# Kernel tuning notes

Hardware: AMD Instinct MI355X
Metric: run time of the kernel (lower is better)

Reference implementation:

```python
import jax, jax.numpy as jnp
import numpy as np

B, S, E, H, D = 2, 2048, 1024, 16, 64  # batch, seq(=max_seq_len), embed_dim, heads, atten_dim


def setup_inputs() -> dict:
    key = jax.random.key(0)
    ks = jax.random.split(key, 9)
    s = 0.02
    return {
        "x": jax.random.normal(ks[0], (B, S, E), jnp.float32),
        "Wq": jax.random.normal(ks[1], (H, E, D), jnp.float32) * s,
        "Wk": jax.random.normal(ks[2], (H, E, D), jnp.float32) * s,
        "Wv": jax.random.normal(ks[3], (H, E, D), jnp.float32) * s,
        "bq": jax.random.normal(ks[4], (H, D), jnp.float32) * s,
        "bk": jax.random.normal(ks[5], (H, D), jnp.float32) * s,
        "bv": jax.random.normal(ks[6], (H, D), jnp.float32) * s,
        "Wp": jax.random.normal(ks[7], (H * D, E), jnp.float32) * s,
        "bp": jax.random.normal(ks[8], (E,), jnp.float32) * s,
    }


def reference(x, Wq, Wk, Wv, bq, bk, bv, Wp, bp):
    scale = jnp.sqrt(jnp.float32(D))
    # per-head projections, all heads at once: [B,H,S,D]
    q = jnp.einsum("bse,hed->bhsd", x, Wq) + bq[:, None, :]
    k = jnp.einsum("bse,hed->bhsd", x, Wk) + bk[:, None, :]
    v = jnp.einsum("bse,hed->bhsd", x, Wv) + bv[:, None, :]
    # causal scores [B,H,S,S], additive -inf mask above diagonal (as in the buffer)
    score = jnp.einsum("bhsd,bhtd->bhst", q, k) / scale
    mask = jnp.triu(jnp.full((S, S), -jnp.inf, jnp.float32), k=1)
    score = score + mask
    probs = jax.nn.softmax(score, axis=-1)
    attn = jnp.einsum("bhst,bhtd->bhsd", probs, v)
    # concat heads -> [B,S,H*D], then projection + ReLU
    concat = attn.transpose(0, 2, 1, 3).reshape(B, S, H * D)
    out = jax.nn.relu(concat @ Wp + bp)
    return out
```

## Files before the change

kernel.cpp:

```cpp
#include <hip/hip_runtime.h>

#define S_LEN 2048
#define E_DIM 1024
#define H_NUM 16
#define D_DIM 64

typedef unsigned short u16;
using bf16x8 = __attribute__((ext_vector_type(8))) short;
using f32x4  = __attribute__((ext_vector_type(4))) float;

#define MFMA16(A, B, C) __builtin_amdgcn_mfma_f32_16x16x32_bf16(A, B, C, 0, 0, 0)

__device__ __forceinline__ u16 f2bf(float f) {
    unsigned u = __float_as_uint(f);
    u += 0x7fffu + ((u >> 16) & 1u);
    return (u16)(u >> 16);
}
__device__ __forceinline__ f32x4 fzero4() { f32x4 z; z[0]=0.f; z[1]=0.f; z[2]=0.f; z[3]=0.f; return z; }

__device__ __forceinline__ void gll16(const u16* g, u16* l) {
    __builtin_amdgcn_global_load_lds(
        (const __attribute__((address_space(1))) void*)g,
        (__attribute__((address_space(3))) void*)l, 16, 0, 0);
}

__global__ __launch_bounds__(256) void cvt_bf16(const float* __restrict__ in, u16* __restrict__ outp, int n) {
    int i4 = (blockIdx.x * 256 + threadIdx.x) * 4;
    if (i4 < n) {
        float4 f = *(const float4*)(in + i4);
        unsigned lo = (unsigned)f2bf(f.x) | ((unsigned)f2bf(f.y) << 16);
        unsigned hi = (unsigned)f2bf(f.z) | ((unsigned)f2bf(f.w) << 16);
        uint2 p; p.x = lo; p.y = hi;
        *(uint2*)(outp + i4) = p;
    }
}

__device__ __forceinline__ void cvt_t_tile(const float* __restrict__ bin, u16* __restrict__ bout,
                                           int R, int C, int r0, int c0) {
    __shared__ float t[64][65];
    const int tid = threadIdx.x;
    const int lr = tid >> 2, lc = (tid & 3) * 16;

    const float* src = bin + (size_t)(r0 + lr) * C + c0 + lc;
    #pragma unroll
    for (int j = 0; j < 4; j++) {
        float4 f = *(const float4*)(src + j * 4);
        t[lr][lc + j * 4 + 0] = f.x; t[lr][lc + j * 4 + 1] = f.y;
        t[lr][lc + j * 4 + 2] = f.z; t[lr][lc + j * 4 + 3] = f.w;
    }
    __syncthreads();

    u16* dst = bout + (size_t)(c0 + lr) * R + r0 + lc;
    u16 vals[16];
    #pragma unroll
    for (int i = 0; i < 16; i++) vals[i] = f2bf(t[lc + i][lr]);
    uint4 pa, pb;
    pa.x = vals[0] | (vals[1] << 16);  pa.y = vals[2] | (vals[3] << 16);
    pa.z = vals[4] | (vals[5] << 16);  pa.w = vals[6] | (vals[7] << 16);
    pb.x = vals[8] | (vals[9] << 16);  pb.y = vals[10] | (vals[11] << 16);
    pb.z = vals[12] | (vals[13] << 16); pb.w = vals[14] | (vals[15] << 16);
    *(uint4*)dst = pa;
    *(uint4*)(dst + 8) = pb;
}

__global__ __launch_bounds__(256) void cvt_bf16_t(const float* __restrict__ in, u16* __restrict__ outp,
                                                  int R, int C) {
    const float* bin = in + (size_t)blockIdx.z * R * C;
    u16* bout = outp + (size_t)blockIdx.z * R * C;
    cvt_t_tile(bin, bout, R, C, blockIdx.y * 64, blockIdx.x * 64);
}

__global__ __launch_bounds__(256) void cvt_w3_t(
    const float* __restrict__ Wq, const float* __restrict__ Wk, const float* __restrict__ Wv,
    u16* __restrict__ wqt, u16* __restrict__ wkt, u16* __restrict__ wvt) {
    const int which = blockIdx.z >> 4, bh = blockIdx.z & 15;
    const float* in = (which == 0) ? Wq : (which == 1) ? Wk : Wv;
    u16* outp = (which == 0) ? wqt : (which == 1) ? wkt : wvt;
    const float* bin = in + (size_t)bh * E_DIM * D_DIM;
    u16* bout = outp + (size_t)bh * E_DIM * D_DIM;
    cvt_t_tile(bin, bout, E_DIM, D_DIM, blockIdx.y * 64, 0);
}

__global__ __launch_bounds__(256) void vt_prep(const u16* __restrict__ v, u16* __restrict__ vt) {
    const int st = blockIdx.x;
    const int bhi = blockIdx.y;
    __shared__ u16 t[64 * 72];
    const int tid = threadIdx.x;
    const int wave = tid >> 6, lane = tid & 63;

    const u16* src = v + (size_t)bhi * S_LEN * D_DIM + (size_t)(st * 64 + lane) * D_DIM + wave * 16;
    uint4 a = *(const uint4*)(src);
    uint4 b = *(const uint4*)(src + 8);
    unsigned w[8] = { a.x, a.y, a.z, a.w, b.x, b.y, b.z, b.w };
    #pragma unroll
    for (int j = 0; j < 8; j++) {
        t[(wave * 16 + 2 * j    ) * 72 + lane] = (u16)(w[j] & 0xffffu);
        t[(wave * 16 + 2 * j + 1) * 72 + lane] = (u16)(w[j] >> 16);
    }
    __syncthreads();

    const int dr = tid >> 2, sc = (tid & 3) * 16;
    u16* dst = vt + (size_t)bhi * D_DIM * S_LEN + (size_t)dr * S_LEN + st * 64 + sc;
    *(uint4*)(dst    ) = *(const uint4*)(&t[dr * 72 + sc    ]);
    *(uint4*)(dst + 8) = *(const uint4*)(&t[dr * 72 + sc + 8]);
}

__global__ __launch_bounds__(256) void qkv_gemm(
    const u16* __restrict__ xb, const u16* __restrict__ wcat,
    const float* __restrict__ bq, const float* __restrict__ bk, const float* __restrict__ bv,
    u16* __restrict__ oq, u16* __restrict__ okk, u16* __restrict__ ov)
{
    const int m0 = blockIdx.x * 128;
    const int n0 = blockIdx.y * 128;

    __shared__ u16 As[128 * 32];
    __shared__ u16 Bs[128 * 32];

    const int tid  = threadIdx.x;
    const int wave = tid >> 6, lane = tid & 63, quad = lane >> 4, l16 = lane & 15;
    const int mh = wave >> 1, nh = wave & 1;

    const int lrow = lane >> 2, lcol = (lane & 3) * 8;
    const u16* aBase = xb   + (size_t)(m0 + wave * 32 + lrow) * E_DIM + lcol;
    const u16* bBase = wcat + (size_t)(n0 + wave * 32 + lrow) * E_DIM + lcol;
    u16* aLds0 = &As[(wave * 32     ) * 32];
    u16* aLds1 = &As[(wave * 32 + 16) * 32];
    u16* bLds0 = &Bs[(wave * 32     ) * 32];
    u16* bLds1 = &Bs[(wave * 32 + 16) * 32];

    f32x4 acc[4][4];
    #pragma unroll
    for (int j = 0; j < 4; j++)
        #pragma unroll
        for (int mi = 0; mi < 4; mi++) acc[j][mi] = fzero4();

    for (int k0 = 0; k0 < E_DIM; k0 += 32) {
        __syncthreads();
        gll16(aBase + k0,                 aLds0);
        gll16(aBase + k0 + 16 * E_DIM,    aLds1);
        gll16(bBase + k0,                 bLds0);
        gll16(bBase + k0 + 16 * E_DIM,    bLds1);
        __syncthreads();

        bf16x8 af[4];
        #pragma unroll
        for (int mi = 0; mi < 4; mi++)
            af[mi] = *(const bf16x8*)(&As[(mh * 64 + mi * 16 + l16) * 32 + quad * 8]);
        #pragma unroll
        for (int j = 0; j < 4; j++) {
            bf16x8 bfv = *(const bf16x8*)(&Bs[(nh * 64 + j * 16 + l16) * 32 + quad * 8]);
            #pragma unroll
            for (int mi = 0; mi < 4; mi++)
                acc[j][mi] = MFMA16(af[mi], bfv, acc[j][mi]);
        }
    }

    u16* outp[3] = { oq, okk, ov };
    const float* biasp[3] = { bq, bk, bv };
    #pragma unroll
    for (int j = 0; j < 4; j++) {
        const int n = n0 + nh * 64 + j * 16 + l16;
        const int t = n >> 10, h = (n >> 6) & 15, d = n & 63;
        float bia = biasp[t][h * D_DIM + d];
        const float scl = (t == 0) ? 0.125f : 1.0f;
        u16* dst = outp[t];
        #pragma unroll
        for (int mi = 0; mi < 4; mi++) {
            #pragma unroll
            for (int r = 0; r < 4; r++) {
                int m = m0 + mh * 64 + mi * 16 + quad * 4 + r;
                int b = m >> 11, s = m & 2047;
                dst[((size_t)(b * H_NUM + h) * S_LEN + s) * D_DIM + d] =
                    f2bf((acc[j][mi][r] + bia) * scl);
            }
        }
    }
}

__global__ __launch_bounds__(256) void attn_fwd(
    const u16* __restrict__ q, const u16* __restrict__ k, const u16* __restrict__ vt,
    u16* __restrict__ concat)
{
    const int p  = blockIdx.x;
    const int qa = p, qb = 31 - p;
    const int h  = blockIdx.y;
    const int bb = blockIdx.z;

    const size_t headoff = (size_t)(bb * H_NUM + h) * S_LEN * D_DIM;
    const u16* qh  = q  + headoff;
    const u16* kh  = k  + headoff;
    const u16* vth = vt + headoff;

    __shared__ u16 Qa[64 * 72];
    __shared__ u16 Qb[64 * 72];
    __shared__ u16 Ks[64 * 72];
    __shared__ u16 Vts[64 * 72];
    __shared__ u16 Ps[4][16 * 72];

    const int tid  = threadIdx.x;
    const int wave = tid >> 6, lane = tid & 63, quad = lane >> 4, l16 = lane & 15;

    const int srow = tid >> 2, scg = tid & 3;

    {
        const u16* qsa = qh + (size_t)(qa * 64 + srow) * D_DIM + scg * 16;
        const u16* qsb = qh + (size_t)(qb * 64 + srow) * D_DIM + scg * 16;
        *(uint4*)(&Qa[srow * 72 + scg * 16    ]) = *(const uint4*)(qsa);
        *(uint4*)(&Qa[srow * 72 + scg * 16 + 8]) = *(const uint4*)(qsa + 8);
        *(uint4*)(&Qb[srow * 72 + scg * 16    ]) = *(const uint4*)(qsb);
        *(uint4*)(&Qb[srow * 72 + scg * 16 + 8]) = *(const uint4*)(qsb + 8);
    }
    __syncthreads();

    bf16x8 bqa0 = *(const bf16x8*)(&Qa[(wave * 16 + l16) * 72 + quad * 8]);
    bf16x8 bqa1 = *(const bf16x8*)(&Qa[(wave * 16 + l16) * 72 + 32 + quad * 8]);
    bf16x8 bqb0 = *(const bf16x8*)(&Qb[(wave * 16 + l16) * 72 + quad * 8]);
    bf16x8 bqb1 = *(const bf16x8*)(&Qb[(wave * 16 + l16) * 72 + 32 + quad * 8]);

    f32x4 oa[4], ob[4];
    #pragma unroll
    for (int nt = 0; nt < 4; nt++) { oa[nt] = fzero4(); ob[nt] = fzero4(); }
    float la = 0.f, lb = 0.f;

    uint4 kA, kB, vA, vB;
    {
        const u16* ksrc = kh + (size_t)srow * D_DIM + scg * 16;
        kA = *(const uint4*)(ksrc); kB = *(const uint4*)(ksrc + 8);
        const u16* vsrc = vth + (size_t)srow * S_LEN + scg * 16;
        vA = *(const uint4*)(vsrc); vB = *(const uint4*)(vsrc + 8);
    }

    const int qga = qa * 64 + wave * 16 + l16;
    const int qgb = qb * 64 + wave * 16 + l16;

    for (int kt = 0; kt <= qb; kt++) {
        __syncthreads();
        *(uint4*)(&Ks[srow * 72 + scg * 16    ]) = kA;
        *(uint4*)(&Ks[srow * 72 + scg * 16 + 8]) = kB;
        *(uint4*)(&Vts[srow * 72 + scg * 16    ]) = vA;
        *(uint4*)(&Vts[srow * 72 + scg * 16 + 8]) = vB;
        __syncthreads();

        if (kt < qb) {
            const u16* ksrc = kh + (size_t)((kt + 1) * 64 + srow) * D_DIM + scg * 16;
            kA = *(const uint4*)(ksrc); kB = *(const uint4*)(ksrc + 8);
            const u16* vsrc = vth + (size_t)srow * S_LEN + (kt + 1) * 64 + scg * 16;
            vA = *(const uint4*)(vsrc); vB = *(const uint4*)(vsrc + 8);
        }

        const bool both = (kt <= qa);

        f32x4 stb[4], sta[4];
        #pragma unroll
        for (int nt = 0; nt < 4; nt++) {
            bf16x8 ak0 = *(const bf16x8*)(&Ks[(nt * 16 + l16) * 72 + quad * 8]);
            bf16x8 ak1 = *(const bf16x8*)(&Ks[(nt * 16 + l16) * 72 + 32 + quad * 8]);
            stb[nt] = fzero4();
            stb[nt] = MFMA16(ak0, bqb0, stb[nt]);
            stb[nt] = MFMA16(ak1, bqb1, stb[nt]);
            if (both) {
                sta[nt] = fzero4();
                sta[nt] = MFMA16(ak0, bqa0, sta[nt]);
                sta[nt] = MFMA16(ak1, bqa1, sta[nt]);
            }
        }

        {
            u16* pw = &Ps[wave][0];
            #pragma unroll
            for (int nt = 0; nt < 4; nt++) {
                float pe[4];
                if (kt == qb) {
                    #pragma unroll
                    for (int r = 0; r < 4; r++) {
                        int kkg = kt * 64 + nt * 16 + quad * 4 + r;
                        pe[r] = (kkg > qgb) ? 0.f : __expf(stb[nt][r]);
                    }
                } else {
                    #pragma unroll
                    for (int r = 0; r < 4; r++) pe[r] = __expf(stb[nt][r]);
                }
                lb += pe[0] + pe[1] + pe[2] + pe[3];
                uint2 pk;
                pk.x = (unsigned)f2bf(pe[0]) | ((unsigned)f2bf(pe[1]) << 16);
                pk.y = (unsigned)f2bf(pe[2]) | ((unsigned)f2bf(pe[3]) << 16);
                *(uint2*)(&pw[l16 * 72 + nt * 16 + quad * 4]) = pk;
            }
            bf16x8 ap0 = *(const bf16x8*)(&Ps[wave][l16 * 72 + quad * 8]);
            bf16x8 ap1 = *(const bf16x8*)(&Ps[wave][l16 * 72 + 32 + quad * 8]);
            #pragma unroll
            for (int nt = 0; nt < 4; nt++) {
                bf16x8 bv0 = *(const bf16x8*)(&Vts[(nt * 16 + l16) * 72 + quad * 8]);
                bf16x8 bv1 = *(const bf16x8*)(&Vts[(nt * 16 + l16) * 72 + 32 + quad * 8]);
                ob[nt] = MFMA16(ap0, bv0, ob[nt]);
                ob[nt] = MFMA16(ap1, bv1, ob[nt]);
            }
        }

        if (both) {
            u16* pw = &Ps[wave][0];
            #pragma unroll
            for (int nt = 0; nt < 4; nt++) {
                float pe[4];
                if (kt == qa) {
                    #pragma unroll
                    for (int r = 0; r < 4; r++) {
                        int kkg = kt * 64 + nt * 16 + quad * 4 + r;
                        pe[r] = (kkg > qga) ? 0.f : __expf(sta[nt][r]);
                    }
                } else {
                    #pragma unroll
                    for (int r = 0; r < 4; r++) pe[r] = __expf(sta[nt][r]);
                }
                la += pe[0] + pe[1] + pe[2] + pe[3];
                uint2 pk;
                pk.x = (unsigned)f2bf(pe[0]) | ((unsigned)f2bf(pe[1]) << 16);
                pk.y = (unsigned)f2bf(pe[2]) | ((unsigned)f2bf(pe[3]) << 16);
                *(uint2*)(&pw[l16 * 72 + nt * 16 + quad * 4]) = pk;
            }
            bf16x8 ap0 = *(const bf16x8*)(&Ps[wave][l16 * 72 + quad * 8]);
            bf16x8 ap1 = *(const bf16x8*)(&Ps[wave][l16 * 72 + 32 + quad * 8]);
            #pragma unroll
            for (int nt = 0; nt < 4; nt++) {
                bf16x8 bv0 = *(const bf16x8*)(&Vts[(nt * 16 + l16) * 72 + quad * 8]);
                bf16x8 bv1 = *(const bf16x8*)(&Vts[(nt * 16 + l16) * 72 + 32 + quad * 8]);
                oa[nt] = MFMA16(ap0, bv0, oa[nt]);
                oa[nt] = MFMA16(ap1, bv1, oa[nt]);
            }
        }
    }

    lb += __shfl_xor(lb, 16); lb += __shfl_xor(lb, 32);
    la += __shfl_xor(la, 16); la += __shfl_xor(la, 32);

    #pragma unroll
    for (int r = 0; r < 4; r++) {
        const int srcl = quad * 4 + r;
        float lbr = __shfl(lb, srcl);
        float lar = __shfl(la, srcl);
        int sqa = qa * 64 + wave * 16 + quad * 4 + r;
        int sqb = qb * 64 + wave * 16 + quad * 4 + r;
        #pragma unroll
        for (int nt = 0; nt < 4; nt++) {
            concat[((size_t)(bb * S_LEN + sqa)) * E_DIM + h * D_DIM + nt * 16 + l16] =
                f2bf(oa[nt][r] / lar);
            concat[((size_t)(bb * S_LEN + sqb)) * E_DIM + h * D_DIM + nt * 16 + l16] =
                f2bf(ob[nt][r] / lbr);
        }
    }
}

__global__ __launch_bounds__(256) void out_proj(
    const u16* __restrict__ concat, const u16* __restrict__ wpt,
    const float* __restrict__ bp, float* __restrict__ out)
{
    const int m0 = blockIdx.x * 128;
    const int n0 = blockIdx.y * 128;

    __shared__ u16 As[128 * 40];
    __shared__ u16 Bs[128 * 40];

    const int tid  = threadIdx.x;
    const int wave = tid >> 6, lane = tid & 63, quad = lane >> 4, l16 = lane & 15;
    const int mh = wave >> 1, nh = wave & 1;

    const int arow = tid >> 1, acol = (tid & 1) * 16;

    const u16* aptr = concat + (size_t)(m0 + arow) * E_DIM + acol;
    const u16* bptr = wpt + (size_t)(n0 + arow) * E_DIM + acol;

    f32x4 acc[4][4];
    #pragma unroll
    for (int j = 0; j < 4; j++)
        #pragma unroll
        for (int mi = 0; mi < 4; mi++) acc[j][mi] = fzero4();

    uint4 pA0, pA1, pB0, pB1;
    pA0 = *(const uint4*)(aptr);     pA1 = *(const uint4*)(aptr + 8);
    pB0 = *(const uint4*)(bptr);     pB1 = *(const uint4*)(bptr + 8);

    for (int k0 = 0; k0 < E_DIM; k0 += 32) {
        __syncthreads();
        *(uint4*)(&As[arow * 40 + acol    ]) = pA0;
        *(uint4*)(&As[arow * 40 + acol + 8]) = pA1;
        *(uint4*)(&Bs[arow * 40 + acol    ]) = pB0;
        *(uint4*)(&Bs[arow * 40 + acol + 8]) = pB1;
        __syncthreads();

        if (k0 + 32 < E_DIM) {
            pA0 = *(const uint4*)(aptr + k0 + 32);  pA1 = *(const uint4*)(aptr + k0 + 40);
            pB0 = *(const uint4*)(bptr + k0 + 32);  pB1 = *(const uint4*)(bptr + k0 + 40);
        }

        bf16x8 af[4];
        #pragma unroll
        for (int mi = 0; mi < 4; mi++)
            af[mi] = *(const bf16x8*)(&As[(mh * 64 + mi * 16 + l16) * 40 + quad * 8]);
        #pragma unroll
        for (int j = 0; j < 4; j++) {
            bf16x8 bfv = *(const bf16x8*)(&Bs[(nh * 64 + j * 16 + l16) * 40 + quad * 8]);
            #pragma unroll
            for (int mi = 0; mi < 4; mi++)
                acc[j][mi] = MFMA16(af[mi], bfv, acc[j][mi]);
        }
    }

    #pragma unroll
    for (int j = 0; j < 4; j++) {
        int n = n0 + nh * 64 + j * 16 + l16;
        float bia = bp[n];
        #pragma unroll
        for (int mi = 0; mi < 4; mi++) {
            #pragma unroll
            for (int r = 0; r < 4; r++) {
                int m = m0 + mh * 64 + mi * 16 + quad * 4 + r;
                out[(size_t)m * E_DIM + n] = fmaxf(acc[j][mi][r] + bia, 0.f);
            }
        }
    }
}

extern "C" void kernel_launch(void* const* d_in, const int* in_sizes, int n_in,
                              void* d_out, int out_size, void* d_ws, size_t ws_size,
                              hipStream_t stream)
{
    (void)in_sizes; (void)n_in; (void)out_size; (void)ws_size;
    const float* x  = (const float*)d_in[0];
    const float* Wq = (const float*)d_in[1];
    const float* Wk = (const float*)d_in[2];
    const float* Wv = (const float*)d_in[3];
    const float* bq = (const float*)d_in[4];
    const float* bk = (const float*)d_in[5];
    const float* bv = (const float*)d_in[6];
    const float* Wp = (const float*)d_in[7];
    const float* bp = (const float*)d_in[8];
    float* out = (float*)d_out;

    const size_t QKV_ELEMS = (size_t)2 * H_NUM * S_LEN * D_DIM;
    const size_t W_ELEMS   = (size_t)H_NUM * E_DIM * D_DIM;

    u16* q   = (u16*)d_ws;
    u16* k   = q   + QKV_ELEMS;
    u16* v   = k   + QKV_ELEMS;
    u16* cc  = v   + QKV_ELEMS;
    u16* xb  = cc  + QKV_ELEMS;
    u16* wqt = xb  + QKV_ELEMS;
    u16* wkt = wqt + W_ELEMS;
    u16* wvt = wkt + W_ELEMS;
    u16* wpt = wvt + W_ELEMS;
    u16* vtr = xb;

    cvt_bf16<<<dim3(4096), 256, 0, stream>>>(x, xb, (int)QKV_ELEMS);
    cvt_w3_t<<<dim3(1, 16, 48), 256, 0, stream>>>(Wq, Wk, Wv, wqt, wkt, wvt);
    cvt_bf16_t<<<dim3(16, 16, 1), 256, 0, stream>>>(Wp, wpt, H_NUM * D_DIM, E_DIM);

    qkv_gemm<<<dim3(32, 24), 256, 0, stream>>>(xb, wqt, bq, bk, bv, q, k, v);
    vt_prep<<<dim3(32, 32), 256, 0, stream>>>(v, vtr);
    attn_fwd<<<dim3(16, 16, 2), 256, 0, stream>>>(q, k, vtr, cc);
    out_proj<<<dim3(32, 8), 256, 0, stream>>>(cc, wpt, bp, out);
}
```

Before: 200.4 us.

## Split attention KV range across two blocks and merge partials in out_proj

Attention now splits each query tile's causal KV range into two halves processed by separate blocks (split-K). This doubles the grid and launch_bounds requests 4 blocks per SM for higher occupancy. Unnormalised bf16 partial outputs and row sums go to workspace, and out_proj merges and normalises them while loading its A operand. The kernel also uses exp2 with log2e folded into the Q scale, a truncating bf16 pack for P, XOR-swizzled LDS, and double-buffered async global->LDS loads for K/V. The cost is extra workspace traffic for the partials, added merge arithmetic in out_proj, and some rounding of partial results to bf16.

```diff
diff --git a/kernel.cpp b/kernel.cpp
--- a/kernel.cpp
+++ b/kernel.cpp
@@ -16,6 +16,10 @@
     u += 0x7fffu + ((u >> 16) & 1u);
     return (u16)(u >> 16);
 }
+__device__ __forceinline__ unsigned pack_bf16_tr(float lo, float hi) {
+    return (__float_as_uint(lo) >> 16) | (__float_as_uint(hi) & 0xffff0000u);
+}
+__device__ __forceinline__ float bfu(unsigned u) { return __uint_as_float(u << 16); }
 __device__ __forceinline__ f32x4 fzero4() { f32x4 z; z[0]=0.f; z[1]=0.f; z[2]=0.f; z[3]=0.f; return z; }
 
 __device__ __forceinline__ void gll16(const u16* g, u16* l) {
@@ -155,6 +159,7 @@
         }
     }
 
+    const float QSCL = 0.125f * 1.44269504089f;
     u16* outp[3] = { oq, okk, ov };
     const float* biasp[3] = { bq, bk, bv };
     #pragma unroll
@@ -162,7 +167,7 @@
         const int n = n0 + nh * 64 + j * 16 + l16;
         const int t = n >> 10, h = (n >> 6) & 15, d = n & 63;
         float bia = biasp[t][h * D_DIM + d];
-        const float scl = (t == 0) ? 0.125f : 1.0f;
+        const float scl = (t == 0) ? QSCL : 1.0f;
         u16* dst = outp[t];
         #pragma unroll
         for (int mi = 0; mi < 4; mi++) {
@@ -177,12 +182,13 @@
     }
 }
 
-__global__ __launch_bounds__(256) void attn_fwd(
+__global__ __launch_bounds__(256, 4) void attn_split(
     const u16* __restrict__ q, const u16* __restrict__ k, const u16* __restrict__ vt,
-    u16* __restrict__ concat)
+    u16* __restrict__ op0, u16* __restrict__ op1,
+    float* __restrict__ ls0, float* __restrict__ ls1)
 {
-    const int p  = blockIdx.x;
-    const int qa = p, qb = 31 - p;
+    const int x = blockIdx.x;
+    const int p = x & 15, half = x >> 4;
     const int h  = blockIdx.y;
     const int bb = blockIdx.z;
 
@@ -191,168 +197,140 @@
     const u16* kh  = k  + headoff;
     const u16* vth = vt + headoff;
 
-    __shared__ u16 Qa[64 * 72];
-    __shared__ u16 Qb[64 * 72];
-    __shared__ u16 Ks[64 * 72];
-    __shared__ u16 Vts[64 * 72];
-    __shared__ u16 Ps[4][16 * 72];
+    u16*   opart = half ? op1 : op0;
+    float* lsum  = half ? ls1 : ls0;
+
+    __shared__ u16 Ks[2][64 * 64];
+    __shared__ u16 Vts[2][64 * 64];
+    __shared__ u16 QP[64 * 64];
 
     const int tid  = threadIdx.x;
     const int wave = tid >> 6, lane = tid & 63, quad = lane >> 4, l16 = lane & 15;
-
     const int srow = tid >> 2, scg = tid & 3;
 
-    {
-        const u16* qsa = qh + (size_t)(qa * 64 + srow) * D_DIM + scg * 16;
-        const u16* qsb = qh + (size_t)(qb * 64 + srow) * D_DIM + scg * 16;
-        *(uint4*)(&Qa[srow * 72 + scg * 16    ]) = *(const uint4*)(qsa);
-        *(uint4*)(&Qa[srow * 72 + scg * 16 + 8]) = *(const uint4*)(qsa + 8);
-        *(uint4*)(&Qb[srow * 72 + scg * 16    ]) = *(const uint4*)(qsb);
-        *(uint4*)(&Qb[srow * 72 + scg * 16 + 8]) = *(const uint4*)(qsb + 8);
-    }
-    __syncthreads();
-
-    bf16x8 bqa0 = *(const bf16x8*)(&Qa[(wave * 16 + l16) * 72 + quad * 8]);
-    bf16x8 bqa1 = *(const bf16x8*)(&Qa[(wave * 16 + l16) * 72 + 32 + quad * 8]);
-    bf16x8 bqb0 = *(const bf16x8*)(&Qb[(wave * 16 + l16) * 72 + quad * 8]);
-    bf16x8 bqb1 = *(const bf16x8*)(&Qb[(wave * 16 + l16) * 72 + 32 + quad * 8]);
-
-    f32x4 oa[4], ob[4];
-    #pragma unroll
-    for (int nt = 0; nt < 4; nt++) { oa[nt] = fzero4(); ob[nt] = fzero4(); }
-    float la = 0.f, lb = 0.f;
-
-    uint4 kA, kB, vA, vB;
-    {
-        const u16* ksrc = kh + (size_t)srow * D_DIM + scg * 16;
-        kA = *(const uint4*)(ksrc); kB = *(const uint4*)(ksrc + 8);
-        const u16* vsrc = vth + (size_t)srow * S_LEN + scg * 16;
-        vA = *(const uint4*)(vsrc); vB = *(const uint4*)(vsrc + 8);
-    }
-
-    const int qga = qa * 64 + wave * 16 + l16;
-    const int qgb = qb * 64 + wave * 16 + l16;
-
-    for (int kt = 0; kt <= qb; kt++) {
+    const int gr = wave * 8 + (lane >> 3);
+    const int gc = lane & 7;
+    const int cl = gc ^ (gr & 7);
+    const u16* kbase = kh  + (size_t)gr * D_DIM + cl * 8;
+    const u16* vbase = vth + (size_t)gr * S_LEN + cl * 8;
+    u16* kl0[2] = { &Ks[0][wave * 512], &Ks[1][wave * 512] };
+    u16* kl1[2] = { &Ks[0][2048 + wave * 512], &Ks[1][2048 + wave * 512] };
+    u16* vl0[2] = { &Vts[0][wave * 512], &Vts[1][wave * 512] };
+    u16* vl1[2] = { &Vts[0][2048 + wave * 512], &Vts[1][2048 + wave * 512] };
+
+    const int sx_lo = ((quad    ) ^ (l16 & 7)) * 8;
+    const int sx_hi = ((quad + 4) ^ (l16 & 7)) * 8;
+    int psw[4];
+    #pragma unroll
+    for (int nt = 0; nt < 4; nt++)
+        psw[nt] = wave * 1024 + l16 * 64 + (((nt * 2 + (quad >> 1)) ^ (l16 & 7)) * 8) + (quad & 1) * 4;
+
+    const int qw = wave * 16 + l16;
+
+    #pragma unroll 1
+    for (int seg = 0; seg < 2; seg++) {
+        const int qt = seg ? (31 - p) : p;
+        const int n  = qt + 1;
+        const int r0 = half ? ((n + 1) >> 1) : 0;
+        const int r1 = half ? n : ((n + 1) >> 1);
+        const int nIt = r1 - r0;
+
         __syncthreads();
-        *(uint4*)(&Ks[srow * 72 + scg * 16    ]) = kA;
-        *(uint4*)(&Ks[srow * 72 + scg * 16 + 8]) = kB;
-        *(uint4*)(&Vts[srow * 72 + scg * 16    ]) = vA;
-        *(uint4*)(&Vts[srow * 72 + scg * 16 + 8]) = vB;
-        __syncthreads();
-
-        if (kt < qb) {
-            const u16* ksrc = kh + (size_t)((kt + 1) * 64 + srow) * D_DIM + scg * 16;
-            kA = *(const uint4*)(ksrc); kB = *(const uint4*)(ksrc + 8);
-            const u16* vsrc = vth + (size_t)srow * S_LEN + (kt + 1) * 64 + scg * 16;
-            vA = *(const uint4*)(vsrc); vB = *(const uint4*)(vsrc + 8);
-        }
-
-        const bool both = (kt <= qa);
-
-        f32x4 stb[4], sta[4];
-        #pragma unroll
-        for (int nt = 0; nt < 4; nt++) {
-            bf16x8 ak0 = *(const bf16x8*)(&Ks[(nt * 16 + l16) * 72 + quad * 8]);
-            bf16x8 ak1 = *(const bf16x8*)(&Ks[(nt * 16 + l16) * 72 + 32 + quad * 8]);
-            stb[nt] = fzero4();
-            stb[nt] = MFMA16(ak0, bqb0, stb[nt]);
-            stb[nt] = MFMA16(ak1, bqb1, stb[nt]);
-            if (both) {
-                sta[nt] = fzero4();
-                sta[nt] = MFMA16(ak0, bqa0, sta[nt]);
-                sta[nt] = MFMA16(ak1, bqa1, sta[nt]);
-            }
+        if (nIt > 0) {
+            gll16(kbase + (size_t)r0 * 4096,                       kl0[0]);
+            gll16(kbase + (size_t)r0 * 4096 + 2048,                kl1[0]);
+            gll16(vbase + (size_t)r0 * 64,                         vl0[0]);
+            gll16(vbase + (size_t)r0 * 64 + (size_t)32 * S_LEN,    vl1[0]);
         }
 
         {
-            u16* pw = &Ps[wave][0];
+            const u16* qs = qh + (size_t)(qt * 64 + srow) * D_DIM + scg * 16;
+            *(uint4*)(&QP[srow * 64 + (((scg * 2    ) ^ (srow & 7)) * 8)]) = *(const uint4*)(qs);
+            *(uint4*)(&QP[srow * 64 + (((scg * 2 + 1) ^ (srow & 7)) * 8)]) = *(const uint4*)(qs + 8);
+        }
+        bf16x8 bq0 = *(const bf16x8*)(&QP[(wave * 16 + l16) * 64 + sx_lo]);
+        bf16x8 bq1 = *(const bf16x8*)(&QP[(wave * 16 + l16) * 64 + sx_hi]);
+
+        f32x4 o[4];
+        #pragma unroll
+        for (int nt = 0; nt < 4; nt++) o[nt] = fzero4();
+        float lsv = 0.f;
+
+        const int qg = qt * 64 + qw;
+
+        for (int i = 0; i < nIt; i++) {
+            const int kt = r0 + i;
+            const u16* ksb = &Ks[i & 1][0];
+            const u16* vsb = &Vts[i & 1][0];
+            __syncthreads();
+
+            if (i + 1 < nIt) {
+                const int nb = (i + 1) & 1;
+                gll16(kbase + (size_t)(kt + 1) * 4096,                    kl0[nb]);
+                gll16(kbase + (size_t)(kt + 1) * 4096 + 2048,             kl1[nb]);
+                gll16(vbase + (size_t)(kt + 1) * 64,                      vl0[nb]);
+                gll16(vbase + (size_t)(kt + 1) * 64 + (size_t)32 * S_LEN, vl1[nb]);
+            }
+
+            f32x4 st[4];
+            #pragma unroll
+            for (int nt = 0; nt < 4; nt++) {
+                bf16x8 ak0 = *(const bf16x8*)(&ksb[(nt * 16 + l16) * 64 + sx_lo]);
+                bf16x8 ak1 = *(const bf16x8*)(&ksb[(nt * 16 + l16) * 64 + sx_hi]);
+                st[nt] = fzero4();
+                st[nt] = MFMA16(ak0, bq0, st[nt]);
+                st[nt] = MFMA16(ak1, bq1, st[nt]);
+            }
+
             #pragma unroll
             for (int nt = 0; nt < 4; nt++) {
                 float pe[4];
-                if (kt == qb) {
+                if (kt == qt) {
                     #pragma unroll
                     for (int r = 0; r < 4; r++) {
                         int kkg = kt * 64 + nt * 16 + quad * 4 + r;
-                        pe[r] = (kkg > qgb) ? 0.f : __expf(stb[nt][r]);
+                        pe[r] = (kkg > qg) ? 0.f : exp2f(st[nt][r]);
                     }
                 } else {
                     #pragma unroll
-                    for (int r = 0; r < 4; r++) pe[r] = __expf(stb[nt][r]);
+                    for (int r = 0; r < 4; r++) pe[r] = exp2f(st[nt][r]);
                 }
-                lb += pe[0] + pe[1] + pe[2] + pe[3];
+                lsv += pe[0] + pe[1] + pe[2] + pe[3];
                 uint2 pk;
-                pk.x = (unsigned)f2bf(pe[0]) | ((unsigned)f2bf(pe[1]) << 16);
-                pk.y = (unsigned)f2bf(pe[2]) | ((unsigned)f2bf(pe[3]) << 16);
-                *(uint2*)(&pw[l16 * 72 + nt * 16 + quad * 4]) = pk;
-            }
-            bf16x8 ap0 = *(const bf16x8*)(&Ps[wave][l16 * 72 + quad * 8]);
-            bf16x8 ap1 = *(const bf16x8*)(&Ps[wave][l16 * 72 + 32 + quad * 8]);
+                pk.x = pack_bf16_tr(pe[0], pe[1]);
+                pk.y = pack_bf16_tr(pe[2], pe[3]);
+                *(uint2*)(&QP[psw[nt]]) = pk;
+            }
+
+            bf16x8 ap0 = *(const bf16x8*)(&QP[wave * 1024 + l16 * 64 + sx_lo]);
+            bf16x8 ap1 = *(const bf16x8*)(&QP[wave * 1024 + l16 * 64 + sx_hi]);
             #pragma unroll
             for (int nt = 0; nt < 4; nt++) {
-                bf16x8 bv0 = *(const bf16x8*)(&Vts[(nt * 16 + l16) * 72 + quad * 8]);
-                bf16x8 bv1 = *(const bf16x8*)(&Vts[(nt * 16 + l16) * 72 + 32 + quad * 8]);
-                ob[nt] = MFMA16(ap0, bv0, ob[nt]);
-                ob[nt] = MFMA16(ap1, bv1, ob[nt]);
-            }
-        }
-
-        if (both) {
-            u16* pw = &Ps[wave][0];
-            #pragma unroll
-            for (int nt = 0; nt < 4; nt++) {
-                float pe[4];
-                if (kt == qa) {
-                    #pragma unroll
-                    for (int r = 0; r < 4; r++) {
-                        int kkg = kt * 64 + nt * 16 + quad * 4 + r;
-                        pe[r] = (kkg > qga) ? 0.f : __expf(sta[nt][r]);
-                    }
-                } else {
-                    #pragma unroll
-                    for (int r = 0; r < 4; r++) pe[r] = __expf(sta[nt][r]);
-                }
-                la += pe[0] + pe[1] + pe[2] + pe[3];
-                uint2 pk;
-                pk.x = (unsigned)f2bf(pe[0]) | ((unsigned)f2bf(pe[1]) << 16);
-                pk.y = (unsigned)f2bf(pe[2]) | ((unsigned)f2bf(pe[3]) << 16);
-                *(uint2*)(&pw[l16 * 72 + nt * 16 + quad * 4]) = pk;
-            }
-            bf16x8 ap0 = *(const bf16x8*)(&Ps[wave][l16 * 72 + quad * 8]);
-            bf16x8 ap1 = *(const bf16x8*)(&Ps[wave][l16 * 72 + 32 + quad * 8]);
-            #pragma unroll
-            for (int nt = 0; nt < 4; nt++) {
-                bf16x8 bv0 = *(const bf16x8*)(&Vts[(nt * 16 + l16) * 72 + quad * 8]);
-                bf16x8 bv1 = *(const bf16x8*)(&Vts[(nt * 16 + l16) * 72 + 32 + quad * 8]);
-                oa[nt] = MFMA16(ap0, bv0, oa[nt]);
-                oa[nt] = MFMA16(ap1, bv1, oa[nt]);
-            }
-        }
-    }
-
-    lb += __shfl_xor(lb, 16); lb += __shfl_xor(lb, 32);
-    la += __shfl_xor(la, 16); la += __shfl_xor(la, 32);
-
-    #pragma unroll
-    for (int r = 0; r < 4; r++) {
-        const int srcl = quad * 4 + r;
-        float lbr = __shfl(lb, srcl);
-        float lar = __shfl(la, srcl);
-        int sqa = qa * 64 + wave * 16 + quad * 4 + r;
-        int sqb = qb * 64 + wave * 16 + quad * 4 + r;
+                bf16x8 bv0 = *(const bf16x8*)(&vsb[(nt * 16 + l16) * 64 + sx_lo]);
+                bf16x8 bv1 = *(const bf16x8*)(&vsb[(nt * 16 + l16) * 64 + sx_hi]);
+                o[nt] = MFMA16(ap0, bv0, o[nt]);
+                o[nt] = MFMA16(ap1, bv1, o[nt]);
+            }
+        }
+
+        lsv += __shfl_xor(lsv, 16); lsv += __shfl_xor(lsv, 32);
+        const size_t rowb = (size_t)(bb * H_NUM + h) * S_LEN + qt * 64;
+        if (quad == 0) lsum[rowb + wave * 16 + l16] = lsv;
         #pragma unroll
         for (int nt = 0; nt < 4; nt++) {
-            concat[((size_t)(bb * S_LEN + sqa)) * E_DIM + h * D_DIM + nt * 16 + l16] =
-                f2bf(oa[nt][r] / lar);
-            concat[((size_t)(bb * S_LEN + sqb)) * E_DIM + h * D_DIM + nt * 16 + l16] =
-                f2bf(ob[nt][r] / lbr);
+            #pragma unroll
+            for (int r = 0; r < 4; r++) {
+                opart[(rowb + wave * 16 + quad * 4 + r) * D_DIM + nt * 16 + l16] =
+                    f2bf(o[nt][r]);
+            }
         }
     }
 }
 
 __global__ __launch_bounds__(256) void out_proj(
-    const u16* __restrict__ concat, const u16* __restrict__ wpt,
-    const float* __restrict__ bp, float* __restrict__ out)
+    const u16* __restrict__ op0, const u16* __restrict__ op1,
+    const float* __restrict__ ls0, const float* __restrict__ ls1,
+    const u16* __restrict__ wpt, const float* __restrict__ bp, float* __restrict__ out)
 {
     const int m0 = blockIdx.x * 128;
     const int n0 = blockIdx.y * 128;
@@ -365,8 +343,16 @@
     const int mh = wave >> 1, nh = wave & 1;
 
     const int arow = tid >> 1, acol = (tid & 1) * 16;
-
-    const u16* aptr = concat + (size_t)(m0 + arow) * E_DIM + acol;
+    const int m = m0 + arow, bI = m >> 11, sI = m & 2047;
+    const size_t oprow0 = (size_t)bI * (H_NUM * S_LEN) + sI;
+
+    float inv[16];
+    #pragma unroll
+    for (int hh = 0; hh < 16; hh++) {
+        size_t r = oprow0 + (size_t)hh * S_LEN;
+        inv[hh] = 1.0f / (ls0[r] + ls1[r]);
+    }
+
     const u16* bptr = wpt + (size_t)(n0 + arow) * E_DIM + acol;
 
     f32x4 acc[4][4];
@@ -375,20 +361,49 @@
         #pragma unroll
         for (int mi = 0; mi < 4; mi++) acc[j][mi] = fzero4();
 
-    uint4 pA0, pA1, pB0, pB1;
-    pA0 = *(const uint4*)(aptr);     pA1 = *(const uint4*)(aptr + 8);
-    pB0 = *(const uint4*)(bptr);     pB1 = *(const uint4*)(bptr + 8);
+    uint4 a0, a1, c0, c1, pB0, pB1;
+    {
+        const int e = acol, hh = e >> 6, d0 = e & 63;
+        const u16* p0 = op0 + (oprow0 + (size_t)hh * S_LEN) * D_DIM + d0;
+        const u16* p1 = op1 + (oprow0 + (size_t)hh * S_LEN) * D_DIM + d0;
+        a0 = *(const uint4*)p0; a1 = *(const uint4*)(p0 + 8);
+        c0 = *(const uint4*)p1; c1 = *(const uint4*)(p1 + 8);
+    }
+    pB0 = *(const uint4*)bptr;  pB1 = *(const uint4*)(bptr + 8);
 
     for (int k0 = 0; k0 < E_DIM; k0 += 32) {
         __syncthreads();
-        *(uint4*)(&As[arow * 40 + acol    ]) = pA0;
-        *(uint4*)(&As[arow * 40 + acol + 8]) = pA1;
+        {
+            const int e = k0 + acol, hh = e >> 6;
+            const float iv = inv[hh];
+            unsigned wa[8] = { a0.x, a0.y, a0.z, a0.w, a1.x, a1.y, a1.z, a1.w };
+            unsigned wc[8] = { c0.x, c0.y, c0.z, c0.w, c1.x, c1.y, c1.z, c1.w };
+            u16 vals[16];
+            #pragma unroll
+            for (int j = 0; j < 8; j++) {
+                float lo = (bfu(wa[j] & 0xffffu) + bfu(wc[j] & 0xffffu)) * iv;
+                float hi = (bfu(wa[j] >> 16)     + bfu(wc[j] >> 16))     * iv;
+                vals[2 * j]     = f2bf(lo);
+                vals[2 * j + 1] = f2bf(hi);
+            }
+            uint4 pa, pb;
+            pa.x = vals[0] | (vals[1] << 16);   pa.y = vals[2] | (vals[3] << 16);
+            pa.z = vals[4] | (vals[5] << 16);   pa.w = vals[6] | (vals[7] << 16);
+            pb.x = vals[8] | (vals[9] << 16);   pb.y = vals[10] | (vals[11] << 16);
+            pb.z = vals[12] | (vals[13] << 16); pb.w = vals[14] | (vals[15] << 16);
+            *(uint4*)(&As[arow * 40 + acol    ]) = pa;
+            *(uint4*)(&As[arow * 40 + acol + 8]) = pb;
+        }
         *(uint4*)(&Bs[arow * 40 + acol    ]) = pB0;
         *(uint4*)(&Bs[arow * 40 + acol + 8]) = pB1;
         __syncthreads();
 
         if (k0 + 32 < E_DIM) {
-            pA0 = *(const uint4*)(aptr + k0 + 32);  pA1 = *(const uint4*)(aptr + k0 + 40);
+            const int e = k0 + 32 + acol, hh = e >> 6, d0 = e & 63;
+            const u16* p0 = op0 + (oprow0 + (size_t)hh * S_LEN) * D_DIM + d0;
+            const u16* p1 = op1 + (oprow0 + (size_t)hh * S_LEN) * D_DIM + d0;
+            a0 = *(const uint4*)p0; a1 = *(const uint4*)(p0 + 8);
+            c0 = *(const uint4*)p1; c1 = *(const uint4*)(p1 + 8);
             pB0 = *(const uint4*)(bptr + k0 + 32);  pB1 = *(const uint4*)(bptr + k0 + 40);
         }
 
@@ -413,8 +428,8 @@
         for (int mi = 0; mi < 4; mi++) {
             #pragma unroll
             for (int r = 0; r < 4; r++) {
-                int m = m0 + mh * 64 + mi * 16 + quad * 4 + r;
-                out[(size_t)m * E_DIM + n] = fmaxf(acc[j][mi][r] + bia, 0.f);
+                int mm = m0 + mh * 64 + mi * 16 + quad * 4 + r;
+                out[(size_t)mm * E_DIM + n] = fmaxf(acc[j][mi][r] + bia, 0.f);
             }
         }
     }
@@ -442,13 +457,16 @@
     u16* q   = (u16*)d_ws;
     u16* k   = q   + QKV_ELEMS;
     u16* v   = k   + QKV_ELEMS;
-    u16* cc  = v   + QKV_ELEMS;
-    u16* xb  = cc  + QKV_ELEMS;
+    u16* op1 = v   + QKV_ELEMS;
+    u16* xb  = op1 + QKV_ELEMS;
     u16* wqt = xb  + QKV_ELEMS;
     u16* wkt = wqt + W_ELEMS;
     u16* wvt = wkt + W_ELEMS;
     u16* wpt = wvt + W_ELEMS;
     u16* vtr = xb;
+    u16* op0 = v;
+    float* ls0 = (float*)wqt;
+    float* ls1 = ls0 + (size_t)2 * H_NUM * S_LEN;
 
     cvt_bf16<<<dim3(4096), 256, 0, stream>>>(x, xb, (int)QKV_ELEMS);
     cvt_w3_t<<<dim3(1, 16, 48), 256, 0, stream>>>(Wq, Wk, Wv, wqt, wkt, wvt);
@@ -456,6 +474,6 @@
 
     qkv_gemm<<<dim3(32, 24), 256, 0, stream>>>(xb, wqt, bq, bk, bv, q, k, v);
     vt_prep<<<dim3(32, 32), 256, 0, stream>>>(v, vtr);
-    attn_fwd<<<dim3(16, 16, 2), 256, 0, stream>>>(q, k, vtr, cc);
-    out_proj<<<dim3(32, 8), 256, 0, stream>>>(cc, wpt, bp, out);
-}
+    attn_split<<<dim3(32, 16, 2), 256, 0, stream>>>(q, k, vtr, op0, op1, ls0, ls1);
+    out_proj<<<dim3(32, 8), 256, 0, stream>>>(op0, op1, ls0, ls1, wpt, bp, out);
+}
```

Result: slower. 208.0 us (+3.8%).
